# Kernel tuning notes

Measured on AMD Instinct MI355X. Metric: run time of the kernel, lower is better.

The kernel has to match this reference:

```python
import jax, jax.numpy as jnp
import numpy as np

B, IMG_DIM, H, W = 2, 256, 64, 64
PC_C, PC_D = 16, 16          # voxel_dim = PC_C * PC_D = 256
VOXEL_DIM = PC_C * PC_D
QK_DIM = 256                 # out_channels of img_conv / voxel_conv


def _conv1x1(x, w, b):
    # x: [B, Cin, H, W], w: [Cout, Cin], b: [Cout]  (1x1 conv == per-pixel matmul)
    return jnp.einsum('bchw,oc->bohw', x, w) + b[None, :, None, None]


def setup_inputs() -> dict:
    key = jax.random.key(0)
    ks = jax.random.split(key, 10)
    s = 0.02
    return {
        'img': jax.random.normal(ks[0], (B, IMG_DIM, H, W), jnp.float32),
        'pc': jax.random.normal(ks[1], (B, PC_D, H, W, PC_C), jnp.float32),  # dense() layout [B,D,H,W,C]
        'img_conv_w': jax.random.normal(ks[2], (QK_DIM, IMG_DIM), jnp.float32) * s,
        'img_conv_b': jnp.zeros((QK_DIM,), jnp.float32),
        'voxel_conv_w': jax.random.normal(ks[3], (QK_DIM, VOXEL_DIM), jnp.float32) * s,
        'voxel_conv_b': jnp.zeros((QK_DIM,), jnp.float32),
        'img_v_w': jax.random.normal(ks[4], (IMG_DIM, IMG_DIM), jnp.float32) * s,
        'img_v_b': jnp.zeros((IMG_DIM,), jnp.float32),
        'voxel_v_w': jax.random.normal(ks[5], (VOXEL_DIM, VOXEL_DIM), jnp.float32) * s,
        'voxel_v_b': jnp.zeros((VOXEL_DIM,), jnp.float32),
    }


def reference(img, pc, img_conv_w, img_conv_b, voxel_conv_w, voxel_conv_b,
              img_v_w, img_v_b, voxel_v_w, voxel_v_b):
    b, c_img, h, w = img.shape
    # pc.dense() -> permute(0,4,1,2,3) -> [B, C, D, H, W] -> [B, C*D, H, W]
    pc = jnp.transpose(pc, (0, 4, 1, 2, 3))
    pcb, pcc, pcd, pch, pcw = pc.shape
    pc2 = pc.reshape(pcb, pcc * pcd, pch, pcw)
    n = h * w  # == pch * pcw (required by the bmms)

    img_q = _conv1x1(img, img_conv_w, img_conv_b).reshape(b, QK_DIM, n).transpose(0, 2, 1)  # [B, N, 256]
    pc_k = _conv1x1(pc2, voxel_conv_w, voxel_conv_b).reshape(b, QK_DIM, n)                  # [B, 256, N]
    # unscaled single-head cross attention, softmax over voxel positions
    attn = jax.nn.softmax(jnp.einsum('bnc,bcm->bnm', img_q, pc_k), axis=-1)                 # [B, N_img, N_pc]

    img_v = _conv1x1(img, img_v_w, img_v_b).reshape(b, c_img, n)                            # [B, C_img, N]
    img_v = jnp.einsum('bcn,bmn->bcm', img_v, attn).reshape(b, c_img, h, w)                 # img_v @ attn^T

    pc_v = _conv1x1(pc2, voxel_v_w, voxel_v_b).reshape(b, pcc * pcd, n)                     # [B, C*D, N]
    pc_v = jnp.einsum('bcn,bmn->bcm', pc_v, attn).reshape(b, pcc, pcd, pch, pcw)
    return (img_v, pc_v)
```

## Files before the change

kernel.cpp:

```cpp
#include <hip/hip_runtime.h>
#include <hip/hip_bf16.h>


typedef __hip_bfloat16 bf16;
typedef __attribute__((ext_vector_type(8))) short bf16x8;
typedef __attribute__((ext_vector_type(4))) float f32x4;

#define AS1 __attribute__((address_space(1)))
#define AS3 __attribute__((address_space(3)))

__device__ __forceinline__ void gld_lds16(const bf16* g, bf16* s) {
    __builtin_amdgcn_global_load_lds((const AS1 void*)g, (AS3 void*)s, 16, 0, 0);
}

__device__ __forceinline__ bf16x8 cvt8(const float* __restrict__ p) {
    const float4 a = *(const float4*)p;
    const float4 b = *(const float4*)(p + 4);
    bf16 t[8];
    t[0] = __float2bfloat16(a.x); t[1] = __float2bfloat16(a.y);
    t[2] = __float2bfloat16(a.z); t[3] = __float2bfloat16(a.w);
    t[4] = __float2bfloat16(b.x); t[5] = __float2bfloat16(b.y);
    t[6] = __float2bfloat16(b.z); t[7] = __float2bfloat16(b.w);
    return *(const bf16x8*)t;
}

__global__ __launch_bounds__(256) void proj_kernel(
    const float* __restrict__ img, const float* __restrict__ pc,
    const float* __restrict__ Wq,  const float* __restrict__ bq,
    const float* __restrict__ Wk,  const float* __restrict__ bk,
    const float* __restrict__ Wvi, const float* __restrict__ bvi,
    const float* __restrict__ Wvp, const float* __restrict__ bvp,
    bf16* __restrict__ Qw, bf16* __restrict__ Ktw, bf16* __restrict__ Vall)
{
    __shared__ __align__(16) bf16 XT[64][264];

    const int blk = blockIdx.x;
    const int s   = blk >> 8;
    const int b   = (blk >> 7) & 1;
    const int g   = (blk >> 6) & 1;
    const int n0  = (blk & 63) * 64;
    const int tid = threadIdx.x;

    if (s == 0) {
        const float* src = img + b * 1048576;
        for (int k = 0; k < 16; k++) {
            const int i = tid + k * 256;
            const int cin = i >> 4, nl4 = (i & 15) * 4;
            const float4 v = *(const float4*)&src[cin * 4096 + n0 + nl4];
            XT[nl4 + 0][cin] = __float2bfloat16(v.x);
            XT[nl4 + 1][cin] = __float2bfloat16(v.y);
            XT[nl4 + 2][cin] = __float2bfloat16(v.z);
            XT[nl4 + 3][cin] = __float2bfloat16(v.w);
        }
    } else {
        const float* src = pc + b * 1048576;
        for (int k = 0; k < 16; k++) {
            const int d = k, u = tid;
            const int nl = u >> 2, c4 = (u & 3) * 4;
            const float4 v = *(const float4*)&src[d * 65536 + (n0 + nl) * 16 + c4];
            XT[nl][(c4 + 0) * 16 + d] = __float2bfloat16(v.x);
            XT[nl][(c4 + 1) * 16 + d] = __float2bfloat16(v.y);
            XT[nl][(c4 + 2) * 16 + d] = __float2bfloat16(v.z);
            XT[nl][(c4 + 3) * 16 + d] = __float2bfloat16(v.w);
        }
    }
    __syncthreads();

    const float* W = s ? (g ? Wvp : Wk) : (g ? Wvi : Wq);
    const float* Bv = s ? (g ? bvp : bk) : (g ? bvi : bq);

    const int wv = tid >> 6, lane = tid & 63, l16 = lane & 15, quad = lane >> 4;
    const int ob = wv * 64;

    f32x4 acc[4][4] = {};

    for (int ks = 0; ks < 8; ks++) {
        const int k0 = ks * 32;
        bf16x8 af[4], wf[4];
        for (int ti = 0; ti < 4; ti++)
            af[ti] = *(const bf16x8*)&XT[ti * 16 + l16][k0 + quad * 8];
        for (int tj = 0; tj < 4; tj++)
            wf[tj] = cvt8(&W[(ob + tj * 16 + l16) * 256 + k0 + quad * 8]);
        for (int ti = 0; ti < 4; ti++)
            for (int tj = 0; tj < 4; tj++)
                acc[ti][tj] = __builtin_amdgcn_mfma_f32_16x16x32_bf16(af[ti], wf[tj], acc[ti][tj], 0, 0, 0);
    }

    if (g == 0) {
        bf16* D1 = (s ? Ktw : Qw) + b * (4096 * 256);
        for (int tj = 0; tj < 4; tj++) {
            const int o = ob + tj * 16 + l16;
            const float bias = Bv[o];
            for (int ti = 0; ti < 4; ti++) {
                const int nl = ti * 16 + quad * 4;
                for (int r = 0; r < 4; r++)
                    D1[(n0 + nl + r) * 256 + o] = __float2bfloat16(acc[ti][tj][r] + bias);
            }
        }
    } else {
        bf16* D2 = Vall + b * (512 * 4096) + (s ? 256 * 4096 : 0);
        for (int tj = 0; tj < 4; tj++) {
            const int o = ob + tj * 16 + l16;
            const float bias = Bv[o];
            for (int ti = 0; ti < 4; ti++) {
                const int nl = ti * 16 + quad * 4;
                bf16 pv[4];
                for (int r = 0; r < 4; r++)
                    pv[r] = __float2bfloat16(acc[ti][tj][r] + bias);
                *(uint2*)&D2[o * 4096 + n0 + nl] = *(const uint2*)pv;
            }
        }
    }
}

__global__ __launch_bounds__(256, 4) void attn_s_kernel(
    const bf16* __restrict__ Qw, const bf16* __restrict__ Ktw,
    bf16* __restrict__ Pt, float* __restrict__ Lpart)
{
    __shared__ __align__(16) bf16 smem[2][8192];

    const int b  = blockIdx.z;
    const int q0 = blockIdx.y * 128;
    const int p0 = blockIdx.x * 128;
    const bf16* Aq = Qw  + b * (4096 * 256);
    const bf16* Ak = Ktw + b * (4096 * 256);

    const int tid = threadIdx.x;
    const int wv = tid >> 6, lane = tid & 63, l16 = lane & 15, quad = lane >> 4;
    const int wr = wv >> 1, wc = wv & 1;

    int aoff[4], boff[4];
    for (int t = 0; t < 4; t++) {
        const int rowa = wr * 64 + t * 16 + l16;
        aoff[t] = rowa * 32 + (quad ^ ((rowa >> 1) & 3)) * 8;
        const int rowb = wc * 64 + t * 16 + l16;
        boff[t] = rowb * 32 + (quad ^ ((rowb >> 1) & 3)) * 8;
    }

    const int arow0 = tid >> 2;
    const int kswz = ((tid & 3) ^ ((arow0 >> 1) & 3)) * 8;
    const bf16* Ag0 = Ak + (p0 + arow0) * 256 + kswz;
    const bf16* Ag1 = Ak + (p0 + 64 + arow0) * 256 + kswz;
    const bf16* Bg0 = Aq + (q0 + arow0) * 256 + kswz;
    const bf16* Bg1 = Aq + (q0 + 64 + arow0) * 256 + kswz;

    f32x4 acc[4][4] = {};

#define SSTAGE(buf, ks)                                                 \
    do {                                                                \
        const int _k = (ks) * 32;                                       \
        bf16* _s = &smem[(buf)][0];                                     \
        gld_lds16(Ag0 + _k, _s + tid * 8);                              \
        gld_lds16(Ag1 + _k, _s + 2048 + tid * 8);                       \
        gld_lds16(Bg0 + _k, _s + 4096 + tid * 8);                       \
        gld_lds16(Bg1 + _k, _s + 6144 + tid * 8);                       \
    } while (0)

    SSTAGE(0, 0);
    int cur = 0;
    for (int ks = 0; ks < 8; ks++) {
        if (ks + 1 < 8) {
            SSTAGE(cur ^ 1, ks + 1);
            asm volatile("s_waitcnt vmcnt(4)" ::: "memory");
        } else {
            asm volatile("s_waitcnt vmcnt(0)" ::: "memory");
        }
        __builtin_amdgcn_s_barrier();
        __builtin_amdgcn_sched_barrier(0);

        const bf16* As_ = &smem[cur][0];
        const bf16* Bs_ = &smem[cur][4096];
        bf16x8 af[4], bfr[4];
        for (int t = 0; t < 4; t++) af[t]  = *(const bf16x8*)&As_[aoff[t]];
        for (int t = 0; t < 4; t++) bfr[t] = *(const bf16x8*)&Bs_[boff[t]];
        __builtin_amdgcn_s_setprio(1);
        for (int ti = 0; ti < 4; ti++)
            for (int tj = 0; tj < 4; tj++)
                acc[ti][tj] = __builtin_amdgcn_mfma_f32_16x16x32_bf16(af[ti], bfr[tj], acc[ti][tj], 0, 0, 0);
        __builtin_amdgcn_s_setprio(0);

        asm volatile("s_waitcnt lgkmcnt(0)" ::: "memory");
        __builtin_amdgcn_s_barrier();
        cur ^= 1;
    }
#undef SSTAGE

    bf16* Pdst = Pt + (size_t)b * 4096 * 4096;
    const int strip = blockIdx.x * 2 + wr;
    for (int tj = 0; tj < 4; tj++) {
        const int q = q0 + wc * 64 + tj * 16 + l16;
        float partial = 0.0f;
        for (int ti = 0; ti < 4; ti++) {
            const int p = p0 + wr * 64 + ti * 16 + quad * 4;
            bf16 pv[4];
            for (int r = 0; r < 4; r++) {
                const float e = __expf(fminf(acc[ti][tj][r], 80.0f));
                partial += e;
                pv[r] = __float2bfloat16(e);
            }
            *(uint2*)&Pdst[(size_t)q * 4096 + p] = *(const uint2*)pv;
        }
        partial += __shfl_xor(partial, 16);
        partial += __shfl_xor(partial, 32);
        if (lane < 16)
            Lpart[(size_t)(b * 4096 + q) * 64 + strip] = partial;
    }
}

__global__ __launch_bounds__(256) void lred_kernel(
    const float* __restrict__ Lpart, float* __restrict__ Linv)
{
    const int row = blockIdx.x * 256 + threadIdx.x;
    const float4* lp = (const float4*)&Lpart[(size_t)row * 64];
    float s = 0.0f;
    for (int i = 0; i < 16; i++) {
        const float4 v = lp[i];
        s += v.x + v.y + v.z + v.w;
    }
    Linv[row] = 1.0f / fmaxf(s, 1e-30f);
}

__global__ __launch_bounds__(512, 2) void attn_o_kernel(
    const bf16* __restrict__ Vall, const bf16* __restrict__ Pt,
    const float* __restrict__ Linv, float* __restrict__ out)
{
    __shared__ __align__(16) bf16 smem[2][4][8192];

    const int orig = blockIdx.x;
    const int L = (orig & 7) * 32 + (orig >> 3);
    const int b   = L >> 7;
    const int rem = L & 127;
    const int c0  = (rem & 3) * 128;
    const int q0  = (rem >> 2) * 128;

    const bf16* A = Vall + (size_t)b * 512 * 4096;
    const bf16* B = Pt   + (size_t)b * 4096 * 4096;

    const int tid = threadIdx.x;
    const int grp = tid >> 8;
    const int t8  = tid & 255;
    const int wv = t8 >> 6, lane = t8 & 63, l16 = lane & 15, quad = lane >> 4;
    const int wr = wv >> 1, wc = wv & 1;

    int aoff[4], boff[4];
    for (int t = 0; t < 4; t++) {
        const int rowa = wr * 64 + t * 16 + l16;
        aoff[t] = rowa * 32 + (quad ^ ((rowa >> 1) & 3)) * 8;
        const int rowb = wc * 64 + t * 16 + l16;
        boff[t] = rowb * 32 + (quad ^ ((rowb >> 1) & 3)) * 8;
    }

    const int arow = t8 >> 2;
    const int kswz = ((t8 & 3) ^ ((arow >> 1) & 3)) * 8;
    const int kb = grp * 2048 + kswz;
    const bf16* Ag0 = A + (c0 + arow) * 4096 + kb;
    const bf16* Ag1 = A + (c0 + 64 + arow) * 4096 + kb;
    const bf16* Bg0 = B + (size_t)(q0 + arow) * 4096 + kb;
    const bf16* Bg1 = B + (size_t)(q0 + 64 + arow) * 4096 + kb;

    f32x4 acc[4][4] = {};

#define STAGE(buf, ks)                                                  \
    do {                                                                \
        const int _k = (ks) * 32;                                       \
        bf16* _s = &smem[grp][(buf)][0];                                \
        gld_lds16(Ag0 + _k, _s + t8 * 8);                               \
        gld_lds16(Ag1 + _k, _s + 2048 + t8 * 8);                        \
        gld_lds16(Bg0 + _k, _s + 4096 + t8 * 8);                        \
        gld_lds16(Bg1 + _k, _s + 6144 + t8 * 8);                        \
    } while (0)

    STAGE(0, 0);
    STAGE(1, 1);
    STAGE(2, 2);
    for (int ks = 0; ks < 64; ks++) {
        if (ks + 3 < 64) {
            STAGE((ks + 3) & 3, ks + 3);
            asm volatile("s_waitcnt vmcnt(12)" ::: "memory");
        } else if (ks + 2 < 64) {
            asm volatile("s_waitcnt vmcnt(8)" ::: "memory");
        } else if (ks + 1 < 64) {
            asm volatile("s_waitcnt vmcnt(4)" ::: "memory");
        } else {
            asm volatile("s_waitcnt vmcnt(0)" ::: "memory");
        }
        __builtin_amdgcn_s_barrier();
        __builtin_amdgcn_sched_barrier(0);

        const bf16* As_ = &smem[grp][ks & 3][0];
        const bf16* Bs_ = &smem[grp][ks & 3][4096];
        bf16x8 af[4], bfr[4];
        for (int t = 0; t < 4; t++) af[t]  = *(const bf16x8*)&As_[aoff[t]];
        for (int t = 0; t < 4; t++) bfr[t] = *(const bf16x8*)&Bs_[boff[t]];
        __builtin_amdgcn_s_setprio(1);
        for (int ti = 0; ti < 4; ti++)
            for (int tj = 0; tj < 4; tj++)
                acc[ti][tj] = __builtin_amdgcn_mfma_f32_16x16x32_bf16(af[ti], bfr[tj], acc[ti][tj], 0, 0, 0);
        __builtin_amdgcn_s_setprio(0);

        asm volatile("s_waitcnt lgkmcnt(0)" ::: "memory");
        __builtin_amdgcn_s_barrier();
    }
#undef STAGE

    __syncthreads();

    float* comb = (float*)&smem[0][0][0];
    if (grp == 0) {
        for (int ti = 0; ti < 4; ti++)
            for (int tj = 0; tj < 4; tj++)
                for (int r = 0; r < 4; r++)
                    comb[(wr * 64 + ti * 16 + quad * 4 + r) * 128 + wc * 64 + tj * 16 + l16]
                        = acc[ti][tj][r];
    }
    __syncthreads();
    if (grp == 1) {
        for (int ti = 0; ti < 4; ti++)
            for (int tj = 0; tj < 4; tj++)
                for (int r = 0; r < 4; r++)
                    comb[(wr * 64 + ti * 16 + quad * 4 + r) * 128 + wc * 64 + tj * 16 + l16]
                        += acc[ti][tj][r];
    }
    __syncthreads();

    const int cl = tid >> 2, qb = (tid & 3) * 32;
    const int c_ = c0 + cl;
    const size_t base = (c_ < 256)
        ? ((size_t)b * 1048576 + (size_t)c_ * 4096)
        : (2097152u + (size_t)b * 1048576 + (size_t)(c_ - 256) * 4096);
    for (int j = 0; j < 8; j++) {
        const float4 v = *(const float4*)&comb[cl * 128 + qb + j * 4];
        const float4 l = *(const float4*)&Linv[b * 4096 + q0 + qb + j * 4];
        float4 o;
        o.x = v.x * l.x; o.y = v.y * l.y; o.z = v.z * l.z; o.w = v.w * l.w;
        *(float4*)&out[base + q0 + qb + j * 4] = o;
    }
}

extern "C" void kernel_launch(void* const* d_in, const int* in_sizes, int n_in,
                              void* d_out, int out_size, void* d_ws, size_t ws_size,
                              hipStream_t stream)
{
    const float* img = (const float*)d_in[0];
    const float* pc  = (const float*)d_in[1];
    const float* Wq  = (const float*)d_in[2];
    const float* bq  = (const float*)d_in[3];
    const float* Wk  = (const float*)d_in[4];
    const float* bk  = (const float*)d_in[5];
    const float* Wvi = (const float*)d_in[6];
    const float* bvi = (const float*)d_in[7];
    const float* Wvp = (const float*)d_in[8];
    const float* bvp = (const float*)d_in[9];

    char* ws = (char*)d_ws;
    bf16*  Qw    = (bf16*)(ws);
    bf16*  Ktw   = (bf16*)(ws + (4ull  << 20));
    bf16*  Vall  = (bf16*)(ws + (8ull  << 20));
    bf16*  Pt    = (bf16*)(ws + (16ull << 20));
    float* Lpart = (float*)(ws + (80ull << 20));
    float* Linv  = (float*)(ws + (82ull << 20));

    proj_kernel<<<512, 256, 0, stream>>>(img, pc, Wq, bq, Wk, bk,
                                         Wvi, bvi, Wvp, bvp, Qw, Ktw, Vall);
    attn_s_kernel<<<dim3(32, 32, 2), 256, 0, stream>>>(Qw, Ktw, Pt, Lpart);
    lred_kernel<<<32, 256, 0, stream>>>(Lpart, Linv);
    attn_o_kernel<<<256, 512, 0, stream>>>(Vall, Pt, Linv, (float*)d_out);
}
```

Baseline: 189.8 us.

## Store P matrix in 128x128 tiled layout via LDS-staged transpose

Measured after the change: 190.4 us. About the same (+0.3%).

```diff
diff --git a/kernel.cpp b/kernel.cpp
--- a/kernel.cpp
+++ b/kernel.cpp
@@ -185,25 +185,37 @@
     }
 #undef SSTAGE
 
-    bf16* Pdst = Pt + (size_t)b * 4096 * 4096;
+    __syncthreads();
+
+    bf16* T = &smem[0][0];
     const int strip = blockIdx.x * 2 + wr;
     for (int tj = 0; tj < 4; tj++) {
-        const int q = q0 + wc * 64 + tj * 16 + l16;
+        const int ql = wc * 64 + tj * 16 + l16;
+        const int sw = (ql & 7) << 3;
         float partial = 0.0f;
         for (int ti = 0; ti < 4; ti++) {
-            const int p = p0 + wr * 64 + ti * 16 + quad * 4;
+            const int pb = wr * 64 + ti * 16 + quad * 4;
             bf16 pv[4];
             for (int r = 0; r < 4; r++) {
                 const float e = __expf(fminf(acc[ti][tj][r], 80.0f));
                 partial += e;
                 pv[r] = __float2bfloat16(e);
             }
-            *(uint2*)&Pdst[(size_t)q * 4096 + p] = *(const uint2*)pv;
+            *(uint2*)&T[ql * 128 + (pb ^ sw)] = *(const uint2*)pv;
         }
         partial += __shfl_xor(partial, 16);
         partial += __shfl_xor(partial, 32);
         if (lane < 16)
-            Lpart[(size_t)(b * 4096 + q) * 64 + strip] = partial;
+            Lpart[(size_t)(b * 4096 + q0 + ql) * 64 + strip] = partial;
+    }
+    __syncthreads();
+
+    bf16* Ptile = Pt + (size_t)((b * 32 + (q0 >> 7)) * 32 + (p0 >> 7)) * 16384;
+    for (int j = 0; j < 8; j++) {
+        const int qr = wv * 32 + j * 4 + (lane >> 4);
+        const int pcm = (lane & 15) * 8;
+        const bf16x8 v = *(const bf16x8*)&T[qr * 128 + (pcm ^ ((qr & 7) << 3))];
+        *(bf16x8*)&Ptile[qr * 128 + pcm] = v;
     }
 }
 
@@ -233,8 +245,8 @@
     const int c0  = (rem & 3) * 128;
     const int q0  = (rem >> 2) * 128;
 
-    const bf16* A = Vall + (size_t)b * 512 * 4096;
-    const bf16* B = Pt   + (size_t)b * 4096 * 4096;
+    const bf16* A  = Vall + (size_t)b * 512 * 4096;
+    const bf16* Bt = Pt + (size_t)((b * 32 + (q0 >> 7)) * 32) * 16384;
 
     const int tid = threadIdx.x;
     const int grp = tid >> 8;
@@ -252,22 +264,21 @@
 
     const int arow = t8 >> 2;
     const int kswz = ((t8 & 3) ^ ((arow >> 1) & 3)) * 8;
-    const int kb = grp * 2048 + kswz;
-    const bf16* Ag0 = A + (c0 + arow) * 4096 + kb;
-    const bf16* Ag1 = A + (c0 + 64 + arow) * 4096 + kb;
-    const bf16* Bg0 = B + (size_t)(q0 + arow) * 4096 + kb;
-    const bf16* Bg1 = B + (size_t)(q0 + 64 + arow) * 4096 + kb;
+    const bf16* Ag0 = A + (c0 + arow) * 4096 + kswz;
+    const bf16* Ag1 = A + (c0 + 64 + arow) * 4096 + kswz;
 
     f32x4 acc[4][4] = {};
 
 #define STAGE(buf, ks)                                                  \
     do {                                                                \
-        const int _k = (ks) * 32;                                       \
+        const int _kk = grp * 2048 + (ks) * 32;                         \
         bf16* _s = &smem[grp][(buf)][0];                                \
-        gld_lds16(Ag0 + _k, _s + t8 * 8);                               \
-        gld_lds16(Ag1 + _k, _s + 2048 + t8 * 8);                        \
-        gld_lds16(Bg0 + _k, _s + 4096 + t8 * 8);                        \
-        gld_lds16(Bg1 + _k, _s + 6144 + t8 * 8);                        \
+        gld_lds16(Ag0 + _kk, _s + t8 * 8);                              \
+        gld_lds16(Ag1 + _kk, _s + 2048 + t8 * 8);                       \
+        const bf16* _bp = Bt + (size_t)(_kk >> 7) * 16384               \
+                          + arow * 128 + (_kk & 127) + kswz;            \
+        gld_lds16(_bp, _s + 4096 + t8 * 8);                             \
+        gld_lds16(_bp + 8192, _s + 6144 + t8 * 8);                      \
     } while (0)
 
     STAGE(0, 0);
```
